# Kernel optimization log

Hardware: AMD Instinct MI355X
Metric: run time of the kernel (lower is better)

## Reference

```python
import jax, jax.numpy as jnp
import numpy as np

SQRT2 = 1.4142135623730951  # fused_leaky_relu gain
DN = ('NCHW', 'OIHW', 'NCHW')


def _setup_filter():
    # upfirdn2d.setup_filter([1,3,3,1]): separable outer product, normalized to sum 1
    f = jnp.array([1., 3., 3., 1.], dtype=jnp.float32)
    f = f / jnp.sum(f)
    return jnp.outer(f, f)  # [4,4], symmetric so flip is a no-op


def _depthwise_fir(x, f2, pad, down):
    # upfirdn2d: depthwise conv with the 4x4 resample filter
    C = x.shape[1]
    k = jnp.broadcast_to(f2[None, None], (C, 1, 4, 4)).astype(x.dtype)
    return jax.lax.conv_general_dilated(
        x, k, window_strides=(down, down),
        padding=[(pad, pad), (pad, pad)],
        feature_group_count=C, dimension_numbers=DN)


def _conv(x, w, stride, pad):
    return jax.lax.conv_general_dilated(
        x, w, window_strides=(stride, stride),
        padding=[(pad, pad), (pad, pad)], dimension_numbers=DN)


def _act(x):
    # fused_leaky_relu with no bias: leaky_relu(x, 0.2) * sqrt(2)
    return jax.nn.leaky_relu(x, negative_slope=0.2) * SQRT2


def setup_inputs() -> dict:
    key = jax.random.key(0)
    k1, k2, k3, k4 = jax.random.split(key, 4)
    N, Cin, Cout, H = 16, 256, 512, 64
    return {
        'latents_in': jax.random.normal(k1, (N, Cin, H, H), dtype=jnp.float32),
        'w_conv': jax.random.normal(k2, (Cin, Cin, 3, 3), dtype=jnp.float32),
        'w_down': jax.random.normal(k3, (Cout, Cin, 3, 3), dtype=jnp.float32),
        'w_skip': jax.random.normal(k4, (Cout, Cin, 1, 1), dtype=jnp.float32),
    }


def reference(latents_in, w_conv, w_down, w_skip):
    f2 = _setup_filter()
    Cin = w_conv.shape[1]
    g3 = 1.0 / np.sqrt(Cin * 9)   # weight_gain for 3x3 convs
    g1 = 1.0 / np.sqrt(Cin)       # weight_gain for 1x1 skip conv

    y = latents_in
    # self.conv: 3x3, pad 1, stride 1, no bias, fused leaky relu
    x = _act(_conv(y, w_conv * g3, stride=1, pad=1))
    # self.conv_down: FIR lowpass (pad 2) then 3x3 conv stride 2 (conv2d_resample down=2)
    x = _depthwise_fir(x, f2, pad=2, down=1)          # [N,Cin,H+1,H+1]
    out = _act(_conv(x, w_down * g3, stride=2, pad=0))  # [N,Cout,H/2,H/2]
    # skip path: downsample2d(y) then 1x1 conv (no bias) + act
    skip = _depthwise_fir(y, f2, pad=1, down=2)       # [N,Cin,H/2,H/2]
    skip = _act(_conv(skip, w_skip * g1, stride=1, pad=0))
    return skip + out
```

## Files before the change

### kernel.cpp

```cpp
#include <hip/hip_runtime.h>
#include <hip/hip_bf16.h>
#include <stdint.h>


typedef __bf16 bf8v __attribute__((ext_vector_type(8)));
typedef float  f4   __attribute__((ext_vector_type(4)));

#define G3F (1.0f / 48.0f)
#define G1F (1.0f / 16.0f)
#define SQRT2F 1.4142135623730951f

__device__ __forceinline__ float actf(float v) {
    return (v > 0.0f ? v : 0.2f * v) * SQRT2F;
}
__device__ __forceinline__ unsigned short f2bu(float f) {
    __hip_bfloat16 h = __float2bfloat16(f);
    return *reinterpret_cast<unsigned short*>(&h);
}
__device__ __forceinline__ bf8v ld8(const __hip_bfloat16* p) {
    return *reinterpret_cast<const bf8v*>(p);
}
__device__ __forceinline__ void llds16(const __hip_bfloat16* g, void* l) {
    __builtin_amdgcn_global_load_lds(
        (const __attribute__((address_space(1))) unsigned int*)g,
        (__attribute__((address_space(3))) unsigned int*)l, 16, 0, 0);
}

__global__ __launch_bounds__(256) void p_misc(__hip_bfloat16* __restrict__ xb,
                                              __hip_bfloat16* __restrict__ zbuf,
                                              const float* __restrict__ wconv,
                                              __hip_bfloat16* __restrict__ wA,
                                              const float* __restrict__ wdown,
                                              __hip_bfloat16* __restrict__ wD,
                                              const float* __restrict__ wskip,
                                              __hip_bfloat16* __restrict__ wst) {
    int b = blockIdx.x, t = threadIdx.x;
    if (b < 256) {
        int idx = b * 256 + t;
        int c8 = idx & 31, side = (idx >> 5) & 1, h = (idx >> 6) & 63, n = idx >> 12;
        int wp = side * 65;
        uint4 z = {0, 0, 0, 0};
        *reinterpret_cast<uint4*>(xb + (((size_t)(n * 64 + h) * 66 + wp) << 8) + c8 * 8) = z;
        if (b == 0 && t < 64)
            *reinterpret_cast<uint4*>(zbuf + (t << 3)) = z;
    } else if (b < 544) {
        int idx = (b - 256) * 256 + t;
        int lane = idx & 63;
        int co16 = (idx >> 6) & 15;
        int q    = (idx >> 10) & 7;
        int tp   = idx >> 13;
        int co = co16 * 16 + (lane & 15);
        int ci = q * 32 + (lane >> 4) * 8;
        union { uint4 v; unsigned short h8[8]; } pk;
        #pragma unroll
        for (int e = 0; e < 8; ++e)
            pk.h8[e] = f2bu(wconv[(size_t)(co * 256 + ci + e) * 9 + tp] * G3F);
        *reinterpret_cast<uint4*>(wA + (size_t)idx * 8) = pk.v;
    } else if (b < 1120) {
        int idx = (b - 544) * 256 + t;
        int lane = idx & 63;
        int co16 = (idx >> 6) & 31;
        int q    = (idx >> 11) & 7;
        int tp   = idx >> 14;
        int co = co16 * 16 + (lane & 15);
        int ci = q * 32 + (lane >> 4) * 8;
        union { uint4 v; unsigned short h8[8]; } pk;
        #pragma unroll
        for (int e = 0; e < 8; ++e)
            pk.h8[e] = f2bu(wdown[(size_t)(co * 256 + ci + e) * 9 + tp] * G3F);
        *reinterpret_cast<uint4*>(wD + (size_t)idx * 8) = pk.v;
    } else {
        int idx = (b - 1120) * 256 + t;
        wst[idx] = __float2bfloat16(wskip[idx] * G1F);
    }
}

__global__ __launch_bounds__(256) void p_xb(const float* __restrict__ lat,
                                            __hip_bfloat16* __restrict__ xb) {
    __shared__ float tile[32][65];
    int bx = blockIdx.x;
    int cic = bx & 7, h = (bx >> 3) & 63, n = bx >> 9;
    int ci0 = cic * 32;
    int t = threadIdx.x;
    {
        int cir = t >> 3, wq = (t & 7) * 8;
        const float* src = lat + (((size_t)(n * 256 + ci0 + cir) * 64 + h) * 64 + wq);
        float4 v0 = *(const float4*)src;
        float4 v1 = *(const float4*)(src + 4);
        tile[cir][wq + 0] = v0.x; tile[cir][wq + 1] = v0.y;
        tile[cir][wq + 2] = v0.z; tile[cir][wq + 3] = v0.w;
        tile[cir][wq + 4] = v1.x; tile[cir][wq + 5] = v1.y;
        tile[cir][wq + 6] = v1.z; tile[cir][wq + 7] = v1.w;
    }
    __syncthreads();
    {
        int w = t >> 2, c8 = (t & 3) * 8;
        union { uint4 q; unsigned short h8[8]; } pk;
        #pragma unroll
        for (int j = 0; j < 8; ++j) pk.h8[j] = f2bu(tile[c8 + j][w]);
        __hip_bfloat16* dst = xb + (((size_t)(n * 64 + h) * 66 + (w + 1)) << 8) + ci0 + c8;
        *reinterpret_cast<uint4*>(dst) = pk.q;
    }
}

__global__ __launch_bounds__(256) void k_fir2n(const __hip_bfloat16* __restrict__ xb,
                                               __hip_bfloat16* __restrict__ s2) {
    int idx = blockIdx.x * 256 + threadIdx.x;
    int c8 = idx & 31, ow = (idx >> 5) & 31, oh = (idx >> 10) & 31, n = idx >> 15;
    const float fk[4] = {0.125f, 0.375f, 0.375f, 0.125f};
    float a8[8];
    #pragma unroll
    for (int e = 0; e < 8; ++e) a8[e] = 0.0f;
    const __hip_bfloat16* src = xb + ((size_t)n * 64 * 66) * 256 + c8 * 8;
    #pragma unroll
    for (int i = 0; i < 4; ++i) {
        int rr = 2 * oh + i - 1;
        if ((unsigned)rr >= 64u) continue;
        #pragma unroll
        for (int j = 0; j < 4; ++j) {
            int wp = 2 * ow + j;
            bf8v v = ld8(src + ((size_t)(rr * 66 + wp) << 8));
            float fw = fk[i] * fk[j];
            #pragma unroll
            for (int e = 0; e < 8; ++e) a8[e] += fw * (float)v[e];
        }
    }
    union { uint4 q; unsigned short h8[8]; } pk;
    #pragma unroll
    for (int e = 0; e < 8; ++e) pk.h8[e] = f2bu(a8[e]);
    *reinterpret_cast<uint4*>(s2 + (((size_t)(n * 1024 + oh * 32 + ow)) << 8) + c8 * 8) = pk.q;
}

__global__ __launch_bounds__(256) void k_skipg(const __hip_bfloat16* __restrict__ s2,
                                               const __hip_bfloat16* __restrict__ wst,
                                               float* __restrict__ out) {
    const int lane = threadIdx.x & 63;
    const int wid  = threadIdx.x >> 6;
    const int wr = wid & 1, wc = wid >> 1;
    const int l15 = lane & 15, g = lane >> 4;

    int raw = blockIdx.x;
    int lg  = (raw & 7) * 64 + (raw >> 3);
    int cot = lg & 3, pxt = lg >> 2;
    int n = pxt >> 3, oh0 = (pxt & 7) * 4;

    f4 acc[4][4];
    #pragma unroll
    for (int m = 0; m < 4; ++m)
        #pragma unroll
        for (int nf = 0; nf < 4; ++nf)
            #pragma unroll
            for (int e = 0; e < 4; ++e) acc[m][nf][e] = 0.0f;

    #pragma unroll
    for (int k = 0; k < 8; ++k) {
        bf8v a_[4], b_[4];
        #pragma unroll
        for (int nf = 0; nf < 4; ++nf) {
            int oh = oh0 + wc * 2 + (nf >> 1);
            int ow = (nf & 1) * 16 + l15;
            b_[nf] = ld8(s2 + (((size_t)(n * 1024 + oh * 32 + ow)) << 8) + k * 32 + g * 8);
        }
        #pragma unroll
        for (int m = 0; m < 4; ++m) {
            int co = cot * 128 + wr * 64 + m * 16 + l15;
            a_[m] = ld8(wst + (size_t)co * 256 + k * 32 + g * 8);
        }
        #pragma unroll
        for (int m = 0; m < 4; ++m)
            #pragma unroll
            for (int nf = 0; nf < 4; ++nf)
                acc[m][nf] = __builtin_amdgcn_mfma_f32_16x16x32_bf16(
                    a_[m], b_[nf], acc[m][nf], 0, 0, 0);
    }
    #pragma unroll
    for (int m = 0; m < 4; ++m)
        #pragma unroll
        for (int nf = 0; nf < 4; ++nf) {
            f4 v = acc[m][nf];
            int oh = oh0 + wc * 2 + (nf >> 1);
            int ow = (nf & 1) * 16 + l15;
            int co = cot * 128 + wr * 64 + m * 16 + 4 * g;
            #pragma unroll
            for (int r = 0; r < 4; ++r)
                out[((size_t)(n * 512 + co + r)) * 1024 + oh * 32 + ow] = actf(v[r]);
        }
}

__global__ __launch_bounds__(256, 4) void k_conv1s(const __hip_bfloat16* __restrict__ xb,
                                                   const __hip_bfloat16* __restrict__ wA,
                                                   const __hip_bfloat16* __restrict__ zbuf,
                                                   __hip_bfloat16* __restrict__ x1) {
    __shared__ uint4 smq[2112];
    char* smc = (char*)smq;
    const int tid  = threadIdx.x;
    const int lane = tid & 63;
    const int wid  = tid >> 6;
    const int wr = wid & 1, wc = wid >> 1;
    const int l15 = lane & 15, g = lane >> 4;

    int raw = blockIdx.x;
    int lg  = (raw & 7) * 128 + (raw >> 3);
    int cot = lg >> 9, pxt = lg & 511;
    int n = pxt >> 5, h0 = (pxt & 31) * 2;
    const size_t nb66 = (size_t)n * 64 * 66 * 256;
    const size_t nb   = (size_t)n * 4096 * 256;
    const char* wAc = (const char*)wA;

    f4 acc[4][4];
    #pragma unroll
    for (int m = 0; m < 4; ++m)
        #pragma unroll
        for (int nf = 0; nf < 4; ++nf)
            #pragma unroll
            for (int e = 0; e < 4; ++e) acc[m][nf][e] = 0.0f;

    #pragma unroll 1
    for (int ch = 0; ch < 4; ++ch) {
        if (ch) __syncthreads();
        for (int li = wid; li < 33; li += 4) {
            int gi = li * 64 + lane;
            int row = (gi >= 1584) ? 3 : (gi >= 1056) ? 2 : (gi >= 528) ? 1 : 0;
            int rem = gi - row * 528;
            int wp = rem >> 3;
            int c8 = (rem & 7) ^ (wp & 7);
            int rc = h0 - 1 + row;
            const __hip_bfloat16* src = ((unsigned)rc < 64u)
                ? xb + nb66 + (((size_t)(rc * 66 + wp)) << 8) + ch * 64 + c8 * 8
                : zbuf + (lane << 3);
            llds16(src, smc + li * 1024);
        }
        __syncthreads();

        auto loadBf = [&](int p, int nf) -> bf8v {
            int tap = p >> 1, qq = p & 1;
            int kh = tap / 3, kw = tap % 3;
            int wp = nf * 16 + l15 + kw;
            int c8r = qq * 4 + g;
            int off = (wc + kh) * 8448 + (wp * 8 + (c8r ^ (wp & 7))) * 16;
            return *(const bf8v*)(smc + off);
        };
        auto loadAf = [&](int p, int m) -> bf8v {
            int tap = p >> 1, q = ch * 2 + (p & 1);
            return *(const bf8v*)(wAc +
                ((size_t)((tap * 8 + q) * 16 + cot * 8 + wr * 4 + m) << 10) +
                (lane << 4));
        };

        bf8v aF[4], bF[4];
        #pragma unroll
        for (int nf = 0; nf < 4; ++nf) bF[nf] = loadBf(0, nf);
        #pragma unroll
        for (int m = 0; m < 4; ++m) aF[m] = loadAf(0, m);

        #pragma unroll
        for (int p = 0; p < 18; ++p) {
            const bool lastp = (p == 17);
            #pragma unroll
            for (int m = 0; m < 3; ++m) {
                #pragma unroll
                for (int nf = 0; nf < 4; ++nf)
                    acc[m][nf] = __builtin_amdgcn_mfma_f32_16x16x32_bf16(
                        aF[m], bF[nf], acc[m][nf], 0, 0, 0);
                if (!lastp) aF[m] = loadAf(p + 1, m);
            }
            #pragma unroll
            for (int nf = 0; nf < 4; ++nf) {
                acc[3][nf] = __builtin_amdgcn_mfma_f32_16x16x32_bf16(
                    aF[3], bF[nf], acc[3][nf], 0, 0, 0);
                if (!lastp) bF[nf] = loadBf(p + 1, nf);
            }
            if (!lastp) aF[3] = loadAf(p + 1, 3);
        }
    }

    __syncthreads();
    #pragma unroll
    for (int m = 0; m < 4; ++m)
        #pragma unroll
        for (int nf = 0; nf < 4; ++nf) {
            int p = wc * 64 + nf * 16 + l15;
            int co4 = wr * 16 + m * 4 + g;
            int co4s = co4 ^ ((p & 15) << 1);
            union { unsigned long long u; unsigned short h4[4]; } pk;
            #pragma unroll
            for (int r = 0; r < 4; ++r) pk.h4[r] = f2bu(actf(acc[m][nf][r]));
            *reinterpret_cast<unsigned long long*>(smc + p * 256 + co4s * 8) = pk.u;
        }
    __syncthreads();
    {
        int p = tid >> 1, coh = tid & 1;
        int hh = h0 + (p >> 6), w = p & 63;
        __hip_bfloat16* dst = x1 + nb + (((size_t)(hh * 64 + w)) << 8) + cot * 128 + coh * 64;
        #pragma unroll
        for (int j = 0; j < 8; ++j) {
            int r2 = coh * 8 + j;
            int co4s = (2 * r2) ^ ((p & 15) << 1);
            uint4 v = *reinterpret_cast<const uint4*>(smc + p * 256 + co4s * 8);
            *reinterpret_cast<uint4*>(dst + j * 8) = v;
        }
    }
}

__global__ __launch_bounds__(256) void k_fir1(const __hip_bfloat16* __restrict__ x1,
                                              __hip_bfloat16* __restrict__ xf) {
    int idx = blockIdx.x * 256 + threadIdx.x;
    int c8 = idx & 31; int rest = idx >> 5;
    int owq = rest % 17; rest /= 17;
    int oh = rest % 65; int n = rest / 65;
    int ow0 = owq * 4; if (ow0 > 61) ow0 = 61;
    int ci = c8 * 8;
    const float fk[4] = {0.125f, 0.375f, 0.375f, 0.125f};
    const __hip_bfloat16* src = x1 + (size_t)n * 4096 * 256 + ci;

    float t[7][8];
    #pragma unroll
    for (int c = 0; c < 7; ++c) {
        #pragma unroll
        for (int e = 0; e < 8; ++e) t[c][e] = 0.0f;
        int col = ow0 - 2 + c;
        if ((unsigned)col >= 64u) continue;
        #pragma unroll
        for (int i = 0; i < 4; ++i) {
            int r = oh + i - 2;
            if ((unsigned)r >= 64u) continue;
            bf8v v = ld8(src + ((size_t)(r * 64 + col) << 8));
            float fw = fk[i];
            #pragma unroll
            for (int e = 0; e < 8; ++e) t[c][e] += fw * (float)v[e];
        }
    }
    #pragma unroll
    for (int o = 0; o < 4; ++o) {
        union { uint4 q; unsigned short h8[8]; } pk;
        #pragma unroll
        for (int e = 0; e < 8; ++e) {
            float s = fk[0] * t[o][e] + fk[1] * t[o + 1][e] +
                      fk[2] * t[o + 2][e] + fk[3] * t[o + 3][e];
            pk.h8[e] = f2bu(s);
        }
        *reinterpret_cast<uint4*>(
            xf + ((size_t)n * 4225 + oh * 65 + ow0 + o) * 256 + ci) = pk.q;
    }
}

__global__ __launch_bounds__(256, 3) void k_downs(const __hip_bfloat16* __restrict__ xf,
                                                  const __hip_bfloat16* __restrict__ wD,
                                                  float* __restrict__ out) {
    __shared__ uint4 smq[2688];
    char* smc = (char*)smq;
    const int tid  = threadIdx.x;
    const int lane = tid & 63;
    const int wid  = tid >> 6;
    const int l15  = lane & 15, g = lane >> 4;

    int raw = blockIdx.x;
    int lg  = (raw & 7) * 128 + (raw >> 3);
    int cot = lg & 3;
    int rest = lg >> 2;
    int n = rest >> 4, oht = rest & 15;
    int r0 = oht * 4;
    const size_t nxf = (size_t)n * 4225 * 256;
    const char* wDc = (const char*)wD;

    f4 acc[2][4];
    #pragma unroll
    for (int m = 0; m < 2; ++m)
        #pragma unroll
        for (int nf = 0; nf < 4; ++nf)
            #pragma unroll
            for (int e = 0; e < 4; ++e) acc[m][nf][e] = 0.0f;

    auto stage = [&](int ch, char* dst) {
        #pragma unroll
        for (int li2 = 0; li2 < 6; ++li2) {
            int li = wid + 4 * li2;
            if (li >= 21) break;
            int gi = li * 64 + lane;
            if (gi > 1319) gi = 1319;
            int row = (gi >= 1056) ? 4 : (gi >= 792) ? 3 : (gi >= 528) ? 2 :
                      (gi >= 264) ? 1 : 0;
            int rem = gi - row * 264;
            int wpair = rem >> 3;
            int t4 = (rem & 7) ^ (wpair & 7);
            int odd = t4 >> 2, c8 = t4 & 3;
            int wp = wpair * 2 + odd; if (wp > 64) wp = 64;
            const __hip_bfloat16* src = xf + nxf +
                (((size_t)((r0 + row) * 65 + wp)) << 8) + ch * 32 + c8 * 8;
            llds16(src, dst + li * 1024);
        }
    };

    stage(0, smc);
    __syncthreads();

    #pragma unroll 1
    for (int ch = 0; ch < 8; ++ch) {
        const char* buf = smc + (ch & 1) * 21504;
        char* nxt       = smc + ((ch + 1) & 1) * 21504;
        if (ch < 7) stage(ch + 1, nxt);

        #pragma unroll
        for (int p = 0; p < 9; ++p) {
            int kh = p / 3, kw = p % 3;
            bf8v b_[4];
            #pragma unroll
            for (int nf = 0; nf < 4; ++nf) {
                int ow = (nf & 1) * 16 + l15;
                int wp = 2 * ow + kw;
                int wpair = wp >> 1, odd = wp & 1;
                int s8 = (g + 4 * odd) ^ (wpair & 7);
                int off = ((2 * (nf >> 1) + kh) * 264 + wpair * 8 + s8) * 16;
                b_[nf] = *(const bf8v*)(buf + off);
            }
            #pragma unroll
            for (int m = 0; m < 2; ++m) {
                bf8v a = *(const bf8v*)(wDc +
                    ((size_t)((p * 8 + ch) * 32 + cot * 8 + wid * 2 + m) << 10) +
                    (lane << 4));
                #pragma unroll
                for (int nf = 0; nf < 4; ++nf)
                    acc[m][nf] = __builtin_amdgcn_mfma_f32_16x16x32_bf16(
                        a, b_[nf], acc[m][nf], 0, 0, 0);
            }
        }
        __syncthreads();
    }

    #pragma unroll
    for (int m = 0; m < 2; ++m)
        #pragma unroll
        for (int nf = 0; nf < 4; ++nf) {
            f4 v = acc[m][nf];
            int oh = oht * 2 + (nf >> 1);
            int ow = (nf & 1) * 16 + l15;
            int co = cot * 128 + wid * 32 + m * 16 + 4 * g;
            #pragma unroll
            for (int r = 0; r < 4; ++r) {
                size_t oi = ((size_t)(n * 512 + co + r)) * 1024 + oh * 32 + ow;
                out[oi] += actf(v[r]);
            }
        }
}

extern "C" void kernel_launch(void* const* d_in, const int* in_sizes, int n_in,
                              void* d_out, int out_size, void* d_ws, size_t ws_size,
                              hipStream_t stream) {
    const float* lat   = (const float*)d_in[0];
    const float* wconv = (const float*)d_in[1];
    const float* wdown = (const float*)d_in[2];
    const float* wskip = (const float*)d_in[3];
    float* out = (float*)d_out;

    char* base = (char*)d_ws;
    __hip_bfloat16* xb   = (__hip_bfloat16*)base;
    __hip_bfloat16* xf   = (__hip_bfloat16*)base;
    __hip_bfloat16* x1   = (__hip_bfloat16*)(base + 34611200);
    __hip_bfloat16* s2   = (__hip_bfloat16*)(base + 34611200);
    __hip_bfloat16* wA   = (__hip_bfloat16*)(base + 68165632);
    __hip_bfloat16* wD   = (__hip_bfloat16*)(base + 69345280);
    __hip_bfloat16* wst  = (__hip_bfloat16*)(base + 71704576);
    __hip_bfloat16* zbuf = (__hip_bfloat16*)(base + 71966720);

    hipLaunchKernelGGL(p_misc, dim3(1632), dim3(256), 0, stream,
                       xb, zbuf, wconv, wA, wdown, wD, wskip, wst);
    hipLaunchKernelGGL(p_xb,    dim3(8192), dim3(256), 0, stream, lat,   xb);
    hipLaunchKernelGGL(k_fir2n, dim3(2048), dim3(256), 0, stream, xb, s2);
    hipLaunchKernelGGL(k_skipg, dim3(512),  dim3(256), 0, stream, s2, wst, out);
    hipLaunchKernelGGL(k_conv1s, dim3(1024), dim3(256), 0, stream, xb, wA, zbuf, x1);
    hipLaunchKernelGGL(k_fir1,  dim3(2210), dim3(256), 0, stream, x1, xf);
    hipLaunchKernelGGL(k_downs, dim3(1024), dim3(256), 0, stream, xf, wD, out);
}
```

Before: 231.1 us.

## Enlarge k_downs tile to 4 output rows, drop LDS double buffering

```diff
diff --git a/kernel.cpp b/kernel.cpp
--- a/kernel.cpp
+++ b/kernel.cpp
@@ -344,42 +344,41 @@
     }
 }
 
-__global__ __launch_bounds__(256, 3) void k_downs(const __hip_bfloat16* __restrict__ xf,
+__global__ __launch_bounds__(256, 4) void k_downs(const __hip_bfloat16* __restrict__ xf,
                                                   const __hip_bfloat16* __restrict__ wD,
                                                   float* __restrict__ out) {
-    __shared__ uint4 smq[2688];
+    __shared__ uint4 smq[2376];
     char* smc = (char*)smq;
     const int tid  = threadIdx.x;
     const int lane = tid & 63;
     const int wid  = tid >> 6;
+    const int wr = wid & 1, wc = wid >> 1;
     const int l15  = lane & 15, g = lane >> 4;
 
     int raw = blockIdx.x;
-    int lg  = (raw & 7) * 128 + (raw >> 3);
-    int cot = lg & 3;
-    int rest = lg >> 2;
-    int n = rest >> 4, oht = rest & 15;
-    int r0 = oht * 4;
+    int lg  = (raw & 7) * 64 + (raw >> 3);
+    int oht = lg & 7;
+    int n   = (lg >> 3) & 15;
+    int cot = lg >> 7;
+    int r0  = oht * 8;
     const size_t nxf = (size_t)n * 4225 * 256;
     const char* wDc = (const char*)wD;
 
-    f4 acc[2][4];
-    #pragma unroll
-    for (int m = 0; m < 2; ++m)
+    f4 acc[4][4];
+    #pragma unroll
+    for (int m = 0; m < 4; ++m)
         #pragma unroll
         for (int nf = 0; nf < 4; ++nf)
             #pragma unroll
             for (int e = 0; e < 4; ++e) acc[m][nf][e] = 0.0f;
 
-    auto stage = [&](int ch, char* dst) {
-        #pragma unroll
-        for (int li2 = 0; li2 < 6; ++li2) {
-            int li = wid + 4 * li2;
-            if (li >= 21) break;
+    #pragma unroll 1
+    for (int ch = 0; ch < 8; ++ch) {
+        if (ch) __syncthreads();
+        for (int li = wid; li < 38; li += 4) {
             int gi = li * 64 + lane;
-            if (gi > 1319) gi = 1319;
-            int row = (gi >= 1056) ? 4 : (gi >= 792) ? 3 : (gi >= 528) ? 2 :
-                      (gi >= 264) ? 1 : 0;
+            if (gi > 2375) gi = 2375;
+            int row = gi / 264;
             int rem = gi - row * 264;
             int wpair = rem >> 3;
             int t4 = (rem & 7) ^ (wpair & 7);
@@ -387,18 +386,9 @@
             int wp = wpair * 2 + odd; if (wp > 64) wp = 64;
             const __hip_bfloat16* src = xf + nxf +
                 (((size_t)((r0 + row) * 65 + wp)) << 8) + ch * 32 + c8 * 8;
-            llds16(src, dst + li * 1024);
-        }
-    };
-
-    stage(0, smc);
-    __syncthreads();
-
-    #pragma unroll 1
-    for (int ch = 0; ch < 8; ++ch) {
-        const char* buf = smc + (ch & 1) * 21504;
-        char* nxt       = smc + ((ch + 1) & 1) * 21504;
-        if (ch < 7) stage(ch + 1, nxt);
+            llds16(src, smc + li * 1024);
+        }
+        __syncthreads();
 
         #pragma unroll
         for (int p = 0; p < 9; ++p) {
@@ -407,16 +397,18 @@
             #pragma unroll
             for (int nf = 0; nf < 4; ++nf) {
                 int ow = (nf & 1) * 16 + l15;
+                int oh_loc = wc * 2 + (nf >> 1);
+                int rr = 2 * oh_loc + kh;
                 int wp = 2 * ow + kw;
                 int wpair = wp >> 1, odd = wp & 1;
                 int s8 = (g + 4 * odd) ^ (wpair & 7);
-                int off = ((2 * (nf >> 1) + kh) * 264 + wpair * 8 + s8) * 16;
-                b_[nf] = *(const bf8v*)(buf + off);
+                int off = rr * 4224 + (wpair * 8 + s8) * 16;
+                b_[nf] = *(const bf8v*)(smc + off);
             }
             #pragma unroll
-            for (int m = 0; m < 2; ++m) {
+            for (int m = 0; m < 4; ++m) {
                 bf8v a = *(const bf8v*)(wDc +
-                    ((size_t)((p * 8 + ch) * 32 + cot * 8 + wid * 2 + m) << 10) +
+                    ((size_t)((p * 8 + ch) * 32 + cot * 8 + wr * 4 + m) << 10) +
                     (lane << 4));
                 #pragma unroll
                 for (int nf = 0; nf < 4; ++nf)
@@ -424,17 +416,16 @@
                         a, b_[nf], acc[m][nf], 0, 0, 0);
             }
         }
-        __syncthreads();
-    }
-
-    #pragma unroll
-    for (int m = 0; m < 2; ++m)
+    }
+
+    #pragma unroll
+    for (int m = 0; m < 4; ++m)
         #pragma unroll
         for (int nf = 0; nf < 4; ++nf) {
             f4 v = acc[m][nf];
-            int oh = oht * 2 + (nf >> 1);
+            int oh = oht * 4 + wc * 2 + (nf >> 1);
             int ow = (nf & 1) * 16 + l15;
-            int co = cot * 128 + wid * 32 + m * 16 + 4 * g;
+            int co = cot * 128 + wr * 64 + m * 16 + 4 * g;
             #pragma unroll
             for (int r = 0; r < 4; ++r) {
                 size_t oi = ((size_t)(n * 512 + co + r)) * 1024 + oh * 32 + ow;
@@ -469,5 +460,5 @@
     hipLaunchKernelGGL(k_skipg, dim3(512),  dim3(256), 0, stream, s2, wst, out);
     hipLaunchKernelGGL(k_conv1s, dim3(1024), dim3(256), 0, stream, xb, wA, zbuf, x1);
     hipLaunchKernelGGL(k_fir1,  dim3(2210), dim3(256), 0, stream, x1, xf);
-    hipLaunchKernelGGL(k_downs, dim3(1024), dim3(256), 0, stream, xf, wD, out);
-}
+    hipLaunchKernelGGL(k_downs, dim3(512),  dim3(256), 0, stream, xf, wD, out);
+}
```

Measured after the change: 298.6 us. 29.2% more time.
